# Optimization experiments

Hardware: AMD Instinct MI355X
Metric: run time of the kernel (lower is better)

Reference implementation:

```python
import jax, jax.numpy as jnp
import numpy as np

IN_DIM, OUT_DIM = 256, 64
N_WNODES, N_PNODES, N_EDGES = 100000, 50000, 1600000


def setup_inputs() -> dict:
    key = jax.random.key(0)
    k_h, k_src, k_dst, k_fc, k_attn = jax.random.split(key, 5)
    h = jax.random.normal(k_h, (N_WNODES, IN_DIM), dtype=jnp.float32)
    edge_src = jax.random.randint(k_src, (N_EDGES,), 0, N_WNODES)
    edge_dst = jax.random.randint(k_dst, (N_EDGES,), 0, N_PNODES)
    W_fc = jax.random.normal(k_fc, (IN_DIM, OUT_DIM), dtype=jnp.float32) / np.sqrt(IN_DIM)
    # attn_fc: Linear(2*out_dim, 1, bias=False) -> weight vector of length 2*OUT_DIM
    W_attn = jax.random.normal(k_attn, (2 * OUT_DIM,), dtype=jnp.float32) / np.sqrt(2 * OUT_DIM)
    return {"h": h, "edge_src": edge_src, "edge_dst": edge_dst,
            "n_pnodes": N_PNODES, "W_fc": W_fc, "W_attn": W_attn}


def reference(h, edge_src, edge_dst, n_pnodes, W_fc, W_attn):
    D = W_fc.shape[1]
    z = h @ W_fc                                  # [Nw, D]
    z_src = z[edge_src]                           # [E, D] gather (memory-bound)
    # In the original, only word nodes get 'z'; DGL zero-fills dst 'z', so the
    # dst half of attn_fc contributes nothing: e = leaky_relu(z_src @ a_src + 0 @ a_dst)
    a_src = W_attn[:D]
    e = jax.nn.leaky_relu(z_src @ a_src)          # [E], slope 0.01 matches torch default
    # reduce_func masks zero-valued scores (DGL mailbox padding) with -1000
    e = jnp.where(e == 0.0, -1000.0, e)
    # segment softmax over incoming edges of each destination node
    e_max = jax.ops.segment_max(e, edge_dst, num_segments=n_pnodes)
    e_max = jnp.where(jnp.isfinite(e_max), e_max, 0.0)  # guard empty segments
    w = jnp.exp(e - e_max[edge_dst])              # [E]
    denom = jax.ops.segment_sum(w, edge_dst, num_segments=n_pnodes)
    alpha = w / jnp.maximum(denom[edge_dst], 1e-20)
    # weighted gather-scatter aggregation: sh[dst] = sum alpha * z_src
    h_out = jax.ops.segment_sum(alpha[:, None] * z_src, edge_dst, num_segments=n_pnodes)
    return h_out                                  # [n_pnodes, D] == h[pnode_id]
```

## Files before the change

kernel.cpp:

```cpp
#include <hip/hip_runtime.h>
#include <hip/hip_bf16.h>
#include <math.h>

#define IN_DIM 256
#define OUT_DIM 64
#define CHUNK_LOG2 12
#define BK_LOG2 7
#define MAXNB 512
#define BCAP 6144

typedef __attribute__((ext_vector_type(8))) short short8v;
typedef __attribute__((ext_vector_type(4))) float f32x4;

__device__ __forceinline__ unsigned short f2bf(float f) {
    unsigned u = __float_as_uint(f);
    unsigned r = (u + 0x7fffu + ((u >> 16) & 1u)) >> 16;
    return (unsigned short)r;
}

__device__ __forceinline__ float bf2f(unsigned short b) {
    return __uint_as_float(((unsigned)b) << 16);
}

__device__ __forceinline__ float edge_score(float x) {
    float e = x > 0.0f ? x : 0.01f * x;
    if (e == 0.0f) e = -1000.0f;
    return e;
}

__device__ __forceinline__ void gload_lds16(const void* g, void* l) {
    __builtin_amdgcn_global_load_lds(
        (const __attribute__((address_space(1))) unsigned int*)g,
        (__attribute__((address_space(3))) unsigned int*)l, 16, 0, 0);
}

__global__ __launch_bounds__(256) void prep_kernel(
    const float* __restrict__ Wfc, short8v* __restrict__ wtf,
    int* __restrict__ bres, int nb)
{
    if (blockIdx.x == 0)
        for (int j = threadIdx.x; j < nb; j += 256) bres[j] = 0;

    const int v = blockIdx.x * 256 + threadIdx.x;
    const int ks = v >> 8;
    const int t = (v >> 6) & 3;
    const int lane = v & 63;
    const int lg = lane >> 4, lr = lane & 15;
    short8v b;
    #pragma unroll
    for (int j = 0; j < 8; ++j) {
        const int k = ks * 32 + lg * 8 + j;
        b[j] = (short)f2bf(Wfc[k * OUT_DIM + t * 16 + lr]);
    }
    wtf[v] = b;
}

__global__ __launch_bounds__(256, 2) void mega_kernel(
    const float* __restrict__ h, const short8v* __restrict__ wtf,
    const float* __restrict__ Wattn, const int* __restrict__ esrc,
    const int* __restrict__ edst, unsigned short* __restrict__ z,
    float* __restrict__ s, int* __restrict__ bres, int* __restrict__ brec,
    int n_rows, int n_edges, int nb, int nchunks)
{
    __shared__ float hl[64 * IN_DIM];
    const int bid = blockIdx.x;
    const int tid = threadIdx.x;

    if (bid < nchunks) {
        int* lcnt = (int*)hl;
        int* lwoff = lcnt + MAXNB;
        const int i0 = bid << CHUNK_LOG2;
        const int i1 = min(i0 + (1 << CHUNK_LOG2), n_edges);
        const bool full = (i1 - i0) == (1 << CHUNK_LOG2);

        int4 s4[4], d4[4];
        if (full) {
            const int4* sp = (const int4*)esrc + (i0 >> 2);
            const int4* dp = (const int4*)edst + (i0 >> 2);
            #pragma unroll
            for (int j = 0; j < 4; ++j) {
                s4[j] = sp[j * 256 + tid];
                d4[j] = dp[j * 256 + tid];
            }
        }

        for (int j = tid; j < nb; j += 256) lcnt[j] = 0;
        __syncthreads();
        if (full) {
            #pragma unroll
            for (int j = 0; j < 4; ++j) {
                atomicAdd(&lcnt[d4[j].x >> BK_LOG2], 1);
                atomicAdd(&lcnt[d4[j].y >> BK_LOG2], 1);
                atomicAdd(&lcnt[d4[j].z >> BK_LOG2], 1);
                atomicAdd(&lcnt[d4[j].w >> BK_LOG2], 1);
            }
        } else {
            for (int i = i0 + tid; i < i1; i += 256)
                atomicAdd(&lcnt[edst[i] >> BK_LOG2], 1);
        }
        __syncthreads();
        for (int j = tid; j < nb; j += 256) {
            const int cv = lcnt[j];
            lwoff[j] = cv ? (j * BCAP + atomicAdd(bres + j, cv)) : 0;
        }
        __syncthreads();
        if (full) {
            #pragma unroll
            for (int j = 0; j < 4; ++j) {
                #define EMIT(dd, ss) { \
                    const int pos = atomicAdd(&lwoff[(dd) >> BK_LOG2], 1); \
                    brec[pos] = (ss) | (((dd) & ((1 << BK_LOG2) - 1)) << 17); }
                EMIT(d4[j].x, s4[j].x)
                EMIT(d4[j].y, s4[j].y)
                EMIT(d4[j].z, s4[j].z)
                EMIT(d4[j].w, s4[j].w)
                #undef EMIT
            }
        } else {
            for (int i = i0 + tid; i < i1; i += 256) {
                const int d = edst[i];
                const int pos = atomicAdd(&lwoff[d >> BK_LOG2], 1);
                brec[pos] = esrc[i] | ((d & ((1 << BK_LOG2) - 1)) << 17);
            }
        }
        return;
    }

    const int gb = bid - nchunks;
    const int lane = tid & 63;
    const int wv = tid >> 6;
    const int lg = lane >> 4;
    const int lr = lane & 15;
    const int row0 = gb * 64;

    #pragma unroll
    for (int i = 0; i < 16; ++i) {
        const int r = wv * 16 + i;
        const int grow = min(row0 + r, n_rows - 1);
        const int lslot = lane ^ (r & 7);
        gload_lds16(h + (size_t)grow * IN_DIM + lslot * 4, hl + r * IN_DIM);
    }

    short8v Bf[8][4];
    #pragma unroll
    for (int ks = 0; ks < 8; ++ks)
        #pragma unroll
        for (int t = 0; t < 4; ++t)
            Bf[ks][t] = wtf[(ks * 4 + t) * 64 + lane];

    float a_attn[4];
    #pragma unroll
    for (int t = 0; t < 4; ++t) a_attn[t] = Wattn[t * 16 + lr];

    asm volatile("s_waitcnt vmcnt(0)" ::: "memory");
    __builtin_amdgcn_sched_barrier(0);

    f32x4 acc[4];
    #pragma unroll
    for (int t = 0; t < 4; ++t) acc[t] = (f32x4){0.f, 0.f, 0.f, 0.f};

    const int rowl = wv * 16 + lr;
    const char* rbase = (const char*)hl + rowl * 1024;
    const int swz = (lr & 7) << 4;

    union AB { short8v v; __hip_bfloat162 h2[4]; };
    #pragma unroll
    for (int ks = 0; ks < 8; ++ks) {
        const int lb = ks * 128 + lg * 32;
        const float4 x0 = *(const float4*)(rbase + (lb ^ swz));
        const float4 x1 = *(const float4*)(rbase + ((lb + 16) ^ swz));
        AB u;
        u.h2[0] = __float22bfloat162_rn(float2{x0.x, x0.y});
        u.h2[1] = __float22bfloat162_rn(float2{x0.z, x0.w});
        u.h2[2] = __float22bfloat162_rn(float2{x1.x, x1.y});
        u.h2[3] = __float22bfloat162_rn(float2{x1.z, x1.w});
        #pragma unroll
        for (int t = 0; t < 4; ++t)
            acc[t] = __builtin_amdgcn_mfma_f32_16x16x32_bf16(u.v, Bf[ks][t], acc[t], 0, 0, 0);
    }

    #pragma unroll
    for (int j = 0; j < 4; ++j) {
        const int row = row0 + wv * 16 + lg * 4 + j;
        const bool ok = row < n_rows;
        float sv = 0.0f;
        #pragma unroll
        for (int t = 0; t < 4; ++t) {
            const float v = acc[t][j];
            if (ok) z[(size_t)row * OUT_DIM + t * 16 + lr] =
                __bfloat16_as_ushort(__float2bfloat16(v));
            sv = fmaf(v, a_attn[t], sv);
        }
        #pragma unroll
        for (int o = 1; o < 16; o <<= 1) sv += __shfl_xor(sv, o);
        if (ok && lr == 0) s[row] = sv;
    }
}

__global__ __launch_bounds__(256) void p2_kernel(
    const int* __restrict__ bres, int* __restrict__ brec,
    int2* __restrict__ oln, int n_pnodes)
{
    __shared__ int srec[BCAP];
    __shared__ int lh[128], lsc[128], lwf[128];
    const int b = blockIdx.x;
    const int tid = threadIdx.x;
    const int base = b * BCAP;
    const int len = min(bres[b], BCAP);

    if (tid < 128) lh[tid] = 0;
    __syncthreads();
    for (int i = tid; i < len; i += 256) {
        const int r = brec[base + i];
        srec[i] = r;
        atomicAdd(&lh[r >> 17], 1);
    }
    __syncthreads();
    if (tid < 128) lsc[tid] = lh[tid];
    __syncthreads();
    for (int d = 1; d < 128; d <<= 1) {
        int v = 0;
        if (tid < 128 && tid >= d) v = lsc[tid - d];
        __syncthreads();
        if (tid < 128) lsc[tid] += v;
        __syncthreads();
    }
    const int d0 = b << BK_LOG2;
    if (tid < 128) {
        const int st = lsc[tid] - lh[tid];
        lwf[tid] = st;
        if (d0 + tid < n_pnodes)
            oln[d0 + tid] = make_int2(base + st, lh[tid]);
    }
    __syncthreads();
    for (int i = tid; i < len; i += 256) {
        const int r = srec[i];
        const int pos = atomicAdd(&lwf[r >> 17], 1);
        brec[base + pos] = r & 0x1FFFF;
    }
}

__global__ __launch_bounds__(256) void segment_kernel(
    const int2* __restrict__ oln, const int* __restrict__ ssrc,
    const float* __restrict__ s, const unsigned short* __restrict__ z,
    float* __restrict__ out, int n_pnodes)
{
    const int p = blockIdx.x * 4 + (threadIdx.x >> 6);
    if (p >= n_pnodes) return;
    const int lane = threadIdx.x & 63;
    const int2 ol = oln[p];
    const int beg = ol.x;
    const int len = ol.y;
    const int end = beg + len;

    if (len == 0) {
        out[(size_t)p * OUT_DIM + lane] = 0.0f;
        return;
    }

    float acc = 0.0f, dsum = 0.0f;

    #define GATH1(tt, wsrc, ssrcv) { \
        float wt = __shfl(wsrc, tt); \
        int st = __shfl(ssrcv, tt); \
        acc = fmaf(wt, bf2f(z[(size_t)st * OUT_DIM + lane]), acc); }
    #define GATH8(tt, wsrc, ssrcv) { \
        float w0 = __shfl(wsrc, tt),     w1 = __shfl(wsrc, tt + 1); \
        float w2 = __shfl(wsrc, tt + 2), w3 = __shfl(wsrc, tt + 3); \
        float w4 = __shfl(wsrc, tt + 4), w5 = __shfl(wsrc, tt + 5); \
        float w6 = __shfl(wsrc, tt + 6), w7 = __shfl(wsrc, tt + 7); \
        int a0 = __shfl(ssrcv, tt),     a1 = __shfl(ssrcv, tt + 1); \
        int a2 = __shfl(ssrcv, tt + 2), a3 = __shfl(ssrcv, tt + 3); \
        int a4 = __shfl(ssrcv, tt + 4), a5 = __shfl(ssrcv, tt + 5); \
        int a6 = __shfl(ssrcv, tt + 6), a7 = __shfl(ssrcv, tt + 7); \
        float z0 = bf2f(z[(size_t)a0 * OUT_DIM + lane]); \
        float z1 = bf2f(z[(size_t)a1 * OUT_DIM + lane]); \
        float z2 = bf2f(z[(size_t)a2 * OUT_DIM + lane]); \
        float z3 = bf2f(z[(size_t)a3 * OUT_DIM + lane]); \
        float z4 = bf2f(z[(size_t)a4 * OUT_DIM + lane]); \
        float z5 = bf2f(z[(size_t)a5 * OUT_DIM + lane]); \
        float z6 = bf2f(z[(size_t)a6 * OUT_DIM + lane]); \
        float z7 = bf2f(z[(size_t)a7 * OUT_DIM + lane]); \
        acc = fmaf(w0, z0, acc); acc = fmaf(w1, z1, acc); \
        acc = fmaf(w2, z2, acc); acc = fmaf(w3, z3, acc); \
        acc = fmaf(w4, z4, acc); acc = fmaf(w5, z5, acc); \
        acc = fmaf(w6, z6, acc); acc = fmaf(w7, z7, acc); }

    if (len <= 64) {
        const bool v = lane < len;
        const int j = beg + (v ? lane : 0);
        const int sr = ssrc[j];
        const float e = v ? edge_score(s[sr]) : -INFINITY;
        float m = e;
        #pragma unroll
        for (int o = 32; o > 0; o >>= 1) m = fmaxf(m, __shfl_xor(m, o));
        float w = v ? __expf(e - m) : 0.0f;
        dsum = w;
        #pragma unroll
        for (int o = 32; o > 0; o >>= 1) dsum += __shfl_xor(dsum, o);

        int t = 0;
        for (; t + 8 <= len; t += 8) GATH8(t, w, sr)
        for (; t < len; ++t) GATH1(t, w, sr)
    } else {
        float m = -INFINITY;
        for (int j = beg + lane; j < end; j += 64)
            m = fmaxf(m, edge_score(s[ssrc[j]]));
        #pragma unroll
        for (int o = 32; o > 0; o >>= 1) m = fmaxf(m, __shfl_xor(m, o));

        for (int c = beg; c < end; c += 64) {
            const int j = c + lane;
            float w = 0.0f;
            int sr = 0;
            if (j < end) {
                sr = ssrc[j];
                w = __expf(edge_score(s[sr]) - m);
            }
            dsum += w;
            const int cn = min(64, end - c);
            int t = 0;
            for (; t + 8 <= cn; t += 8) GATH8(t, w, sr)
            for (; t < cn; ++t) GATH1(t, w, sr)
        }
        #pragma unroll
        for (int o = 32; o > 0; o >>= 1) dsum += __shfl_xor(dsum, o);
    }
    #undef GATH8
    #undef GATH1

    out[(size_t)p * OUT_DIM + lane] = acc / fmaxf(dsum, 1e-20f);
}

extern "C" void kernel_launch(void* const* d_in, const int* in_sizes, int n_in,
                              void* d_out, int out_size, void* d_ws, size_t ws_size,
                              hipStream_t stream)
{
    const float* h     = (const float*)d_in[0];
    const int*   esrc  = (const int*)d_in[1];
    const int*   edst  = (const int*)d_in[2];
    const float* Wfc   = (const float*)d_in[4];
    const float* Wattn = (const float*)d_in[5];
    float* out = (float*)d_out;

    const int n_w = in_sizes[0] / IN_DIM;
    const int n_e = in_sizes[1];
    const int n_p = out_size / OUT_DIM;
    const int nb  = (n_p + (1 << BK_LOG2) - 1) >> BK_LOG2;

    short8v* wtf            = (short8v*)d_ws;
    unsigned short* z       = (unsigned short*)(wtf + 2048);
    float* s                = (float*)(z + (size_t)n_w * OUT_DIM);
    int* brec               = (int*)(s + n_w);
    int2* oln               = (int2*)(brec + (size_t)nb * BCAP);
    int* bres               = (int*)(oln + n_p);

    prep_kernel<<<8, 256, 0, stream>>>(Wfc, wtf, bres, nb);

    const int nchunks = (n_e + (1 << CHUNK_LOG2) - 1) >> CHUNK_LOG2;
    const int gemmb = (n_w + 63) / 64;
    mega_kernel<<<nchunks + gemmb, 256, 0, stream>>>(h, wtf, Wattn, esrc, edst,
                                                     z, s, bres, brec,
                                                     n_w, n_e, nb, nchunks);
    p2_kernel<<<nb, 256, 0, stream>>>(bres, brec, oln, n_p);
    segment_kernel<<<(n_p + 3) / 4, 256, 0, stream>>>(oln, brec, s, z, out, n_p);
}
```

Before: 107.0 us.

## Split GEMM row loads into two K halves and widen p2 blocks

The GEMM part of mega_kernel now stages each wave's 16 rows into LDS in two halves along K. It waits only for the first half (vmcnt(8)) and runs the first four MFMA k-steps while the second half is still arriving, which overlaps global-to-LDS traffic with compute. Separately, p2_kernel launches with 512 threads instead of 256 to speed its bucket scatter loops. The risk is that the vmcnt(8) count depends on exactly how many loads the compiler emits, and the per-wave LDS layout changed.

```diff
diff --git a/kernel.cpp b/kernel.cpp
--- a/kernel.cpp
+++ b/kernel.cpp
@@ -133,13 +133,7 @@
     const int lr = lane & 15;
     const int row0 = gb * 64;
 
-    #pragma unroll
-    for (int i = 0; i < 16; ++i) {
-        const int r = wv * 16 + i;
-        const int grow = min(row0 + r, n_rows - 1);
-        const int lslot = lane ^ (r & 7);
-        gload_lds16(h + (size_t)grow * IN_DIM + lslot * 4, hl + r * IN_DIM);
-    }
+    char* qbase = (char*)hl + wv * 16384;
 
     short8v Bf[8][4];
     #pragma unroll
@@ -152,20 +146,35 @@
     #pragma unroll
     for (int t = 0; t < 4; ++t) a_attn[t] = Wattn[t * 16 + lr];
 
-    asm volatile("s_waitcnt vmcnt(0)" ::: "memory");
+    const int rl_dma = (lane >> 5);
+    const int slot = lane & 31;
+    #pragma unroll
+    for (int hh = 0; hh < 2; ++hh) {
+        #pragma unroll
+        for (int j = 0; j < 8; ++j) {
+            const int rl = wv * 16 + 2 * j + rl_dma;
+            const int rg = min(row0 + rl, n_rows - 1);
+            const int sslot = slot ^ (rl & 7);
+            gload_lds16(h + (size_t)rg * IN_DIM + hh * 128 + sslot * 4,
+                        qbase + hh * 8192 + j * 1024);
+        }
+        if (hh == 0) __builtin_amdgcn_sched_barrier(0);
+    }
     __builtin_amdgcn_sched_barrier(0);
 
+    asm volatile("s_waitcnt vmcnt(8)" ::: "memory");
+    __builtin_amdgcn_sched_barrier(0);
+
     f32x4 acc[4];
     #pragma unroll
     for (int t = 0; t < 4; ++t) acc[t] = (f32x4){0.f, 0.f, 0.f, 0.f};
 
-    const int rowl = wv * 16 + lr;
-    const char* rbase = (const char*)hl + rowl * 1024;
+    const char* rbase = qbase + lr * 512;
     const int swz = (lr & 7) << 4;
 
     union AB { short8v v; __hip_bfloat162 h2[4]; };
     #pragma unroll
-    for (int ks = 0; ks < 8; ++ks) {
+    for (int ks = 0; ks < 4; ++ks) {
         const int lb = ks * 128 + lg * 32;
         const float4 x0 = *(const float4*)(rbase + (lb ^ swz));
         const float4 x1 = *(const float4*)(rbase + ((lb + 16) ^ swz));
@@ -179,6 +188,25 @@
             acc[t] = __builtin_amdgcn_mfma_f32_16x16x32_bf16(u.v, Bf[ks][t], acc[t], 0, 0, 0);
     }
 
+    asm volatile("s_waitcnt vmcnt(0)" ::: "memory");
+    __builtin_amdgcn_sched_barrier(0);
+
+    #pragma unroll
+    for (int ks = 4; ks < 8; ++ks) {
+        const int lb = (ks - 4) * 128 + lg * 32;
+        const char* rb1 = rbase + 8192;
+        const float4 x0 = *(const float4*)(rb1 + (lb ^ swz));
+        const float4 x1 = *(const float4*)(rb1 + ((lb + 16) ^ swz));
+        AB u;
+        u.h2[0] = __float22bfloat162_rn(float2{x0.x, x0.y});
+        u.h2[1] = __float22bfloat162_rn(float2{x0.z, x0.w});
+        u.h2[2] = __float22bfloat162_rn(float2{x1.x, x1.y});
+        u.h2[3] = __float22bfloat162_rn(float2{x1.z, x1.w});
+        #pragma unroll
+        for (int t = 0; t < 4; ++t)
+            acc[t] = __builtin_amdgcn_mfma_f32_16x16x32_bf16(u.v, Bf[ks][t], acc[t], 0, 0, 0);
+    }
+
     #pragma unroll
     for (int j = 0; j < 4; ++j) {
         const int row = row0 + wv * 16 + lg * 4 + j;
@@ -197,7 +225,7 @@
     }
 }
 
-__global__ __launch_bounds__(256) void p2_kernel(
+__global__ __launch_bounds__(512) void p2_kernel(
     const int* __restrict__ bres, int* __restrict__ brec,
     int2* __restrict__ oln, int n_pnodes)
 {
@@ -210,7 +238,7 @@
 
     if (tid < 128) lh[tid] = 0;
     __syncthreads();
-    for (int i = tid; i < len; i += 256) {
+    for (int i = tid; i < len; i += 512) {
         const int r = brec[base + i];
         srec[i] = r;
         atomicAdd(&lh[r >> 17], 1);
@@ -233,7 +261,7 @@
             oln[d0 + tid] = make_int2(base + st, lh[tid]);
     }
     __syncthreads();
-    for (int i = tid; i < len; i += 256) {
+    for (int i = tid; i < len; i += 512) {
         const int r = srec[i];
         const int pos = atomicAdd(&lwf[r >> 17], 1);
         brec[base + pos] = r & 0x1FFFF;
@@ -362,6 +390,6 @@
     mega_kernel<<<nchunks + gemmb, 256, 0, stream>>>(h, wtf, Wattn, esrc, edst,
                                                      z, s, bres, brec,
                                                      n_w, n_e, nb, nchunks);
-    p2_kernel<<<nb, 256, 0, stream>>>(bres, brec, oln, n_p);
+    p2_kernel<<<nb, 512, 0, stream>>>(bres, brec, oln, n_p);
     segment_kernel<<<(n_p + 3) / 4, 256, 0, stream>>>(oln, brec, s, z, out, n_p);
 }
```

Result: no change. 105.0 us (-1.9%).

## Make mega kernel persistent with double-buffered GEMM tiles and looped binning

Applied to the files above, without the earlier changes.

Turns the GEMM plus edge-binning kernel into a persistent grid of 512 blocks of 128 threads. Each block loops over 32-row GEMM tiles, using two LDS buffers so the async load of the next tile overlaps the MFMA work on the current one, then loops over edge-binning chunks. p2_kernel is also widened to 512 threads. The aim is to hide global-load latency and cut launch and tail overhead, but the persistent grid may underfill the device or serialize the binning phase behind the GEMM phase, and the 64KB LDS per block limits occupancy.

```diff
diff --git a/kernel.cpp b/kernel.cpp
--- a/kernel.cpp
+++ b/kernel.cpp
@@ -8,6 +8,7 @@
 #define BK_LOG2 7
 #define MAXNB 512
 #define BCAP 6144
+#define PERSIST 512
 
 typedef __attribute__((ext_vector_type(8))) short short8v;
 typedef __attribute__((ext_vector_type(4))) float f32x4;
@@ -55,91 +56,21 @@
     wtf[v] = b;
 }
 
-__global__ __launch_bounds__(256, 2) void mega_kernel(
+__global__ __launch_bounds__(128) void mega_kernel(
     const float* __restrict__ h, const short8v* __restrict__ wtf,
     const float* __restrict__ Wattn, const int* __restrict__ esrc,
     const int* __restrict__ edst, unsigned short* __restrict__ z,
     float* __restrict__ s, int* __restrict__ bres, int* __restrict__ brec,
-    int n_rows, int n_edges, int nb, int nchunks)
-{
-    __shared__ float hl[64 * IN_DIM];
+    int n_rows, int n_edges, int nb, int nchunks, int gemmtiles)
+{
+    __shared__ __align__(16) char hl[65536];
     const int bid = blockIdx.x;
     const int tid = threadIdx.x;
-
-    if (bid < nchunks) {
-        int* lcnt = (int*)hl;
-        int* lwoff = lcnt + MAXNB;
-        const int i0 = bid << CHUNK_LOG2;
-        const int i1 = min(i0 + (1 << CHUNK_LOG2), n_edges);
-        const bool full = (i1 - i0) == (1 << CHUNK_LOG2);
-
-        int4 s4[4], d4[4];
-        if (full) {
-            const int4* sp = (const int4*)esrc + (i0 >> 2);
-            const int4* dp = (const int4*)edst + (i0 >> 2);
-            #pragma unroll
-            for (int j = 0; j < 4; ++j) {
-                s4[j] = sp[j * 256 + tid];
-                d4[j] = dp[j * 256 + tid];
-            }
-        }
-
-        for (int j = tid; j < nb; j += 256) lcnt[j] = 0;
-        __syncthreads();
-        if (full) {
-            #pragma unroll
-            for (int j = 0; j < 4; ++j) {
-                atomicAdd(&lcnt[d4[j].x >> BK_LOG2], 1);
-                atomicAdd(&lcnt[d4[j].y >> BK_LOG2], 1);
-                atomicAdd(&lcnt[d4[j].z >> BK_LOG2], 1);
-                atomicAdd(&lcnt[d4[j].w >> BK_LOG2], 1);
-            }
-        } else {
-            for (int i = i0 + tid; i < i1; i += 256)
-                atomicAdd(&lcnt[edst[i] >> BK_LOG2], 1);
-        }
-        __syncthreads();
-        for (int j = tid; j < nb; j += 256) {
-            const int cv = lcnt[j];
-            lwoff[j] = cv ? (j * BCAP + atomicAdd(bres + j, cv)) : 0;
-        }
-        __syncthreads();
-        if (full) {
-            #pragma unroll
-            for (int j = 0; j < 4; ++j) {
-                #define EMIT(dd, ss) { \
-                    const int pos = atomicAdd(&lwoff[(dd) >> BK_LOG2], 1); \
-                    brec[pos] = (ss) | (((dd) & ((1 << BK_LOG2) - 1)) << 17); }
-                EMIT(d4[j].x, s4[j].x)
-                EMIT(d4[j].y, s4[j].y)
-                EMIT(d4[j].z, s4[j].z)
-                EMIT(d4[j].w, s4[j].w)
-                #undef EMIT
-            }
-        } else {
-            for (int i = i0 + tid; i < i1; i += 256) {
-                const int d = edst[i];
-                const int pos = atomicAdd(&lwoff[d >> BK_LOG2], 1);
-                brec[pos] = esrc[i] | ((d & ((1 << BK_LOG2) - 1)) << 17);
-            }
-        }
-        return;
-    }
-
-    const int gb = bid - nchunks;
     const int lane = tid & 63;
     const int wv = tid >> 6;
     const int lg = lane >> 4;
     const int lr = lane & 15;
-    const int row0 = gb * 64;
-
-    #pragma unroll
-    for (int i = 0; i < 16; ++i) {
-        const int r = wv * 16 + i;
-        const int grow = min(row0 + r, n_rows - 1);
-        const int lslot = lane ^ (r & 7);
-        gload_lds16(h + (size_t)grow * IN_DIM + lslot * 4, hl + r * IN_DIM);
-    }
+    const int G = gridDim.x;
 
     short8v Bf[8][4];
     #pragma unroll
@@ -152,52 +83,136 @@
     #pragma unroll
     for (int t = 0; t < 4; ++t) a_attn[t] = Wattn[t * 16 + lr];
 
+    char* wbase = hl + wv * 32768;
+    const int swz = (lr & 7) << 4;
+
+    union AB { short8v v; __hip_bfloat162 h2[4]; };
+
+    auto ISSUE = [&](int t, char* dst) {
+        const int rb = t * 32 + wv * 16;
+        #pragma unroll
+        for (int i = 0; i < 16; ++i) {
+            const int rg = min(rb + i, n_rows - 1);
+            const int sslot = lane ^ (i & 7);
+            gload_lds16(h + (size_t)rg * IN_DIM + sslot * 4, dst + i * 1024);
+        }
+    };
+
+    if (bid < gemmtiles) {
+        ISSUE(bid, wbase);
+        ISSUE(min(bid + G, gemmtiles - 1), wbase + 16384);
+        __builtin_amdgcn_sched_barrier(0);
+
+        int cur = 0;
+        for (int t = bid; t < gemmtiles; t += G) {
+            asm volatile("s_waitcnt vmcnt(16)" ::: "memory");
+            __builtin_amdgcn_sched_barrier(0);
+
+            const char* rbase = wbase + cur * 16384 + lr * 1024;
+
+            f32x4 acc[4];
+            #pragma unroll
+            for (int tt = 0; tt < 4; ++tt) acc[tt] = (f32x4){0.f, 0.f, 0.f, 0.f};
+
+            #pragma unroll
+            for (int ks = 0; ks < 8; ++ks) {
+                const int lb = ks * 128 + lg * 32;
+                const float4 x0 = *(const float4*)(rbase + (lb ^ swz));
+                const float4 x1 = *(const float4*)(rbase + ((lb + 16) ^ swz));
+                AB u;
+                u.h2[0] = __float22bfloat162_rn(float2{x0.x, x0.y});
+                u.h2[1] = __float22bfloat162_rn(float2{x0.z, x0.w});
+                u.h2[2] = __float22bfloat162_rn(float2{x1.x, x1.y});
+                u.h2[3] = __float22bfloat162_rn(float2{x1.z, x1.w});
+                #pragma unroll
+                for (int tt = 0; tt < 4; ++tt)
+                    acc[tt] = __builtin_amdgcn_mfma_f32_16x16x32_bf16(u.v, Bf[ks][tt], acc[tt], 0, 0, 0);
+            }
+
+            #pragma unroll
+            for (int j = 0; j < 4; ++j) {
+                const int row = t * 32 + wv * 16 + lg * 4 + j;
+                const bool ok = row < n_rows;
+                float sv = 0.0f;
+                #pragma unroll
+                for (int tt = 0; tt < 4; ++tt) {
+                    const float v = acc[tt][j];
+                    if (ok) z[(size_t)row * OUT_DIM + tt * 16 + lr] =
+                        __bfloat16_as_ushort(__float2bfloat16(v));
+                    sv = fmaf(v, a_attn[tt], sv);
+                }
+                #pragma unroll
+                for (int o = 1; o < 16; o <<= 1) sv += __shfl_xor(sv, o);
+                if (ok && lr == 0) s[row] = sv;
+            }
+            __builtin_amdgcn_sched_barrier(0);
+
+            ISSUE(min(t + 2 * G, gemmtiles - 1), wbase + cur * 16384);
+            __builtin_amdgcn_sched_barrier(0);
+            cur ^= 1;
+        }
+    }
+
     asm volatile("s_waitcnt vmcnt(0)" ::: "memory");
     __builtin_amdgcn_sched_barrier(0);
-
-    f32x4 acc[4];
-    #pragma unroll
-    for (int t = 0; t < 4; ++t) acc[t] = (f32x4){0.f, 0.f, 0.f, 0.f};
-
-    const int rowl = wv * 16 + lr;
-    const char* rbase = (const char*)hl + rowl * 1024;
-    const int swz = (lr & 7) << 4;
-
-    union AB { short8v v; __hip_bfloat162 h2[4]; };
-    #pragma unroll
-    for (int ks = 0; ks < 8; ++ks) {
-        const int lb = ks * 128 + lg * 32;
-        const float4 x0 = *(const float4*)(rbase + (lb ^ swz));
-        const float4 x1 = *(const float4*)(rbase + ((lb + 16) ^ swz));
-        AB u;
-        u.h2[0] = __float22bfloat162_rn(float2{x0.x, x0.y});
-        u.h2[1] = __float22bfloat162_rn(float2{x0.z, x0.w});
-        u.h2[2] = __float22bfloat162_rn(float2{x1.x, x1.y});
-        u.h2[3] = __float22bfloat162_rn(float2{x1.z, x1.w});
-        #pragma unroll
-        for (int t = 0; t < 4; ++t)
-            acc[t] = __builtin_amdgcn_mfma_f32_16x16x32_bf16(u.v, Bf[ks][t], acc[t], 0, 0, 0);
-    }
-
-    #pragma unroll
-    for (int j = 0; j < 4; ++j) {
-        const int row = row0 + wv * 16 + lg * 4 + j;
-        const bool ok = row < n_rows;
-        float sv = 0.0f;
-        #pragma unroll
-        for (int t = 0; t < 4; ++t) {
-            const float v = acc[t][j];
-            if (ok) z[(size_t)row * OUT_DIM + t * 16 + lr] =
-                __bfloat16_as_ushort(__float2bfloat16(v));
-            sv = fmaf(v, a_attn[t], sv);
-        }
-        #pragma unroll
-        for (int o = 1; o < 16; o <<= 1) sv += __shfl_xor(sv, o);
-        if (ok && lr == 0) s[row] = sv;
-    }
-}
-
-__global__ __launch_bounds__(256) void p2_kernel(
+    __syncthreads();
+
+    int* lcnt = (int*)hl;
+    int* lwoff = lcnt + MAXNB;
+    for (int c = bid; c < nchunks; c += G) {
+        const int i0 = c << CHUNK_LOG2;
+        const int i1 = min(i0 + (1 << CHUNK_LOG2), n_edges);
+        const bool full = (i1 - i0) == (1 << CHUNK_LOG2);
+
+        for (int j = tid; j < nb; j += 128) lcnt[j] = 0;
+        __syncthreads();
+
+        if (full) {
+            const int4* dp = (const int4*)edst + (i0 >> 2);
+            for (int q = tid; q < (1 << (CHUNK_LOG2 - 2)); q += 128) {
+                const int4 d = dp[q];
+                atomicAdd(&lcnt[d.x >> BK_LOG2], 1);
+                atomicAdd(&lcnt[d.y >> BK_LOG2], 1);
+                atomicAdd(&lcnt[d.z >> BK_LOG2], 1);
+                atomicAdd(&lcnt[d.w >> BK_LOG2], 1);
+            }
+        } else {
+            for (int i = i0 + tid; i < i1; i += 128)
+                atomicAdd(&lcnt[edst[i] >> BK_LOG2], 1);
+        }
+        __syncthreads();
+        for (int j = tid; j < nb; j += 128) {
+            const int cv = lcnt[j];
+            lwoff[j] = cv ? (j * BCAP + atomicAdd(bres + j, cv)) : 0;
+        }
+        __syncthreads();
+        if (full) {
+            const int4* dp = (const int4*)edst + (i0 >> 2);
+            const int4* sp = (const int4*)esrc + (i0 >> 2);
+            for (int q = tid; q < (1 << (CHUNK_LOG2 - 2)); q += 128) {
+                const int4 d = dp[q];
+                const int4 sv4 = sp[q];
+                #define EMIT(dd, ss) { \
+                    const int pos = atomicAdd(&lwoff[(dd) >> BK_LOG2], 1); \
+                    brec[pos] = (ss) | (((dd) & ((1 << BK_LOG2) - 1)) << 17); }
+                EMIT(d.x, sv4.x)
+                EMIT(d.y, sv4.y)
+                EMIT(d.z, sv4.z)
+                EMIT(d.w, sv4.w)
+                #undef EMIT
+            }
+        } else {
+            for (int i = i0 + tid; i < i1; i += 128) {
+                const int d = edst[i];
+                const int pos = atomicAdd(&lwoff[d >> BK_LOG2], 1);
+                brec[pos] = esrc[i] | ((d & ((1 << BK_LOG2) - 1)) << 17);
+            }
+        }
+        __syncthreads();
+    }
+}
+
+__global__ __launch_bounds__(512) void p2_kernel(
     const int* __restrict__ bres, int* __restrict__ brec,
     int2* __restrict__ oln, int n_pnodes)
 {
@@ -210,7 +225,7 @@
 
     if (tid < 128) lh[tid] = 0;
     __syncthreads();
-    for (int i = tid; i < len; i += 256) {
+    for (int i = tid; i < len; i += 512) {
         const int r = brec[base + i];
         srec[i] = r;
         atomicAdd(&lh[r >> 17], 1);
@@ -233,7 +248,7 @@
             oln[d0 + tid] = make_int2(base + st, lh[tid]);
     }
     __syncthreads();
-    for (int i = tid; i < len; i += 256) {
+    for (int i = tid; i < len; i += 512) {
         const int r = srec[i];
         const int pos = atomicAdd(&lwf[r >> 17], 1);
         brec[base + pos] = r & 0x1FFFF;
@@ -358,10 +373,10 @@
     prep_kernel<<<8, 256, 0, stream>>>(Wfc, wtf, bres, nb);
 
     const int nchunks = (n_e + (1 << CHUNK_LOG2) - 1) >> CHUNK_LOG2;
-    const int gemmb = (n_w + 63) / 64;
-    mega_kernel<<<nchunks + gemmb, 256, 0, stream>>>(h, wtf, Wattn, esrc, edst,
-                                                     z, s, bres, brec,
-                                                     n_w, n_e, nb, nchunks);
-    p2_kernel<<<nb, 256, 0, stream>>>(bres, brec, oln, n_p);
+    const int gemmtiles = (n_w + 31) / 32;
+    mega_kernel<<<PERSIST, 128, 0, stream>>>(h, wtf, Wattn, esrc, edst,
+                                             z, s, bres, brec,
+                                             n_w, n_e, nb, nchunks, gemmtiles);
+    p2_kernel<<<nb, 512, 0, stream>>>(bres, brec, oln, n_p);
     segment_kernel<<<(n_p + 3) / 4, 256, 0, stream>>>(oln, brec, s, z, out, n_p);
 }
```

Result: slower. 110.3 us (+3.1%).
